# Optimization experiments

Hardware: AMD Instinct MI355X
Metric: run time of the kernel (lower is better)

## Reference

```python
import jax, jax.numpy as jnp
import numpy as np

N, K, F, NRBF = 10000, 32, 128, 300
GAMMA = 10.0


def ssp(x):
    # shifted softplus: softplus(x) - log(2)
    return jax.nn.softplus(x) - jnp.log(2.0).astype(x.dtype)


def setup_inputs() -> dict:
    key = jax.random.key(0)
    ks = jax.random.split(key, 12)
    s = lambda fan_in: 1.0 / np.sqrt(fan_in)
    inp = {
        "xyz": jax.random.normal(ks[0], (N, 3), jnp.float32) * 5.0,
        "atomic": jax.random.normal(ks[1], (N, F), jnp.float32),
        "edge_mask": (jax.random.uniform(ks[2], (N, K)) < 0.9).astype(jnp.float32),
        "src": jax.random.randint(ks[3], (N, K), 0, N),
        # pre_conv Linear(F, F) with bias
        "W_pre": jax.random.uniform(ks[4], (F, F), jnp.float32, -s(F), s(F)),
        "b_pre": jax.random.uniform(ks[5], (F,), jnp.float32, -s(F), s(F)),
        # cfconv: Linear(300, F, bias=False), SSP, Linear(F, F, bias=False), SSP
        "W_cf1": jax.random.uniform(ks[6], (NRBF, F), jnp.float32, -s(NRBF), s(NRBF)),
        "W_cf2": jax.random.uniform(ks[7], (F, F), jnp.float32, -s(F), s(F)),
        # post_conv: Linear(F,F), SSP, Linear(F,F)
        "W_post1": jax.random.uniform(ks[8], (F, F), jnp.float32, -s(F), s(F)),
        "b_post1": jax.random.uniform(ks[9], (F,), jnp.float32, -s(F), s(F)),
        "W_post2": jax.random.uniform(ks[10], (F, F), jnp.float32, -s(F), s(F)),
        "b_post2": jax.random.uniform(ks[11], (F,), jnp.float32, -s(F), s(F)),
        "rbf_centers": jnp.linspace(0.1, 30.1, NRBF, dtype=jnp.float32),
    }
    return inp


def reference(xyz, atomic, edge_mask, src, W_pre, b_pre, W_cf1, W_cf2,
              W_post1, b_post1, W_post2, b_post2, rbf_centers):
    pre = atomic @ W_pre + b_pre                       # [N, F]
    nbr_xyz = xyz[src]                                 # gather: [N, K, 3]
    d_ij = jnp.linalg.norm(nbr_xyz - xyz[:, None, :], axis=2, keepdims=True)  # [N, K, 1]
    rbf = jnp.exp(-GAMMA * (d_ij - rbf_centers[None, None, :]) ** 2)          # [N, K, 300]
    filters = ssp(ssp(rbf @ W_cf1) @ W_cf2)            # [N, K, F]
    conv_out = jnp.sum(filters * pre[src] * edge_mask[:, :, None], axis=1)    # [N, F]
    post = ssp(conv_out @ W_post1 + b_post1) @ W_post2 + b_post2
    return atomic + post
```

## Files before the change

### kernel.cpp

```cpp
#include <hip/hip_runtime.h>

#define NATOMS 10000
#define KNB 32
#define FD 128
#define NRBF 300
#define STEPC (30.0f / 299.0f)
#define INVSTEP (299.0f / 30.0f)
#define TROWS 256

typedef short short8 __attribute__((ext_vector_type(8)));
typedef float f32x4 __attribute__((ext_vector_type(4)));
typedef unsigned int u32x4 __attribute__((ext_vector_type(4)));

__device__ __forceinline__ unsigned short f2bf_rne(float f) {
    unsigned int u = __float_as_uint(f);
    u = (u + 0x7fffu + ((u >> 16) & 1u)) >> 16;
    return (unsigned short)u;
}

__device__ __forceinline__ unsigned int pack_bf2(float hi, float lo) {
    return __builtin_amdgcn_perm(__float_as_uint(hi) + 0x8000u,
                                 __float_as_uint(lo) + 0x8000u, 0x07060302u);
}

__device__ __forceinline__ unsigned short f2bf_rhu(float f) {
    return (unsigned short)((__float_as_uint(f) + 0x8000u) >> 16);
}

__device__ __forceinline__ float ssp_fast(float x) {
    float t = __builtin_amdgcn_exp2f(x * 1.44269504f);
    float l = __builtin_amdgcn_logf(1.0f + t);
    return 0.69314718056f * (l - 1.0f);
}

__device__ __forceinline__ float ssp_poly(float x) {
    float u = x * x;
    float p = fmaf(u, 2.1356923e-6f, -2.6351976e-5f);
    p = fmaf(u, p, 3.2552083e-4f);
    p = fmaf(u, p, -5.2083333e-3f);
    p = fmaf(u, p, 0.125f);
    return fmaf(0.5f, x, u * p);
}

__device__ __forceinline__ void gload_lds16(const void* g, void* l) {
    __builtin_amdgcn_global_load_lds(
        (const __attribute__((address_space(1))) unsigned int*)g,
        (__attribute__((address_space(3))) unsigned int*)l, 16, 0, 0);
}

__device__ __forceinline__ short8 rbf_row8(float d, float cg) {
    float t = d - cg;
    t = fminf(3.5f, fmaxf(-3.5f, t));
    float r = __builtin_amdgcn_exp2f(-14.4269504f * t * t);
    float q = __builtin_amdgcn_exp2f((28.8539008f * STEPC) * t
                                     - (14.4269504f * STEPC * STEPC));
    const float QRATIO = 0.81763172f;
    u32x4 p;
#pragma unroll
    for (int jj = 0; jj < 4; ++jj) {
        float v0 = r; r *= q; q *= QRATIO;
        float v1 = r; r *= q; q *= QRATIO;
        p[jj] = pack_bf2(v1, v0);
    }
    return __builtin_bit_cast(short8, p);
}

__global__ __launch_bounds__(256) void prep_pack(
    const float* __restrict__ Wcf1, const float* __restrict__ Wpre,
    const float* __restrict__ Wcf2, const float* __restrict__ Wpost1,
    const float* __restrict__ Wpost2, unsigned short* __restrict__ w1p,
    unsigned short* __restrict__ w4p) {
    int idx = blockIdx.x * 256 + threadIdx.x;
    if (idx < 40960) {
        int j = idx & 7, c = (idx >> 3) & 127, g = (idx >> 10) & 3, kc = idx >> 12;
        int k = kc * 32 + g * 8 + j;
        float v = (k < NRBF) ? Wcf1[k * FD + c] : 0.f;
        w1p[idx] = f2bf_rne(v);
    } else if (idx < 40960 + 65536) {
        int t = idx - 40960;
        int sel = t >> 14;
        int t2 = t & 16383;
        int j = t2 & 7, c = (t2 >> 3) & 127, g = (t2 >> 10) & 3, kc = t2 >> 12;
        int k = kc * 32 + g * 8 + j;
        const float* W = (sel == 0) ? Wpre : (sel == 1) ? Wcf2 : (sel == 2) ? Wpost1 : Wpost2;
        w4p[t] = f2bf_rne(W[k * FD + c]);
    }
}

__global__ __launch_bounds__(256) void pre_and_table(
    const float* __restrict__ X, const unsigned short* __restrict__ Wp,
    const float* __restrict__ bias, unsigned int* __restrict__ preP,
    const unsigned short* __restrict__ w1p, const unsigned short* __restrict__ w2p,
    unsigned int* __restrict__ T) {
    __shared__ unsigned short A2[128][132];
    const int tid = threadIdx.x;
    const int w = tid >> 6, lane = tid & 63, g = lane >> 4, c16 = lane & 15;

    if (blockIdx.x < 157) {
        const int r0 = blockIdx.x * 64 + w * 16;
        f32x4 acc[8];
#pragma unroll
        for (int b = 0; b < 8; ++b) acc[b] = (f32x4){0.f, 0.f, 0.f, 0.f};
        int row = r0 + c16;
        if (row >= NATOMS) row = 0;
#pragma unroll
        for (int kc = 0; kc < 4; ++kc) {
            const float* p0 = X + (size_t)row * FD + kc * 32 + g * 8;
            float4 xa = *(const float4*)p0, xb = *(const float4*)(p0 + 4);
            u32x4 pa;
            pa[0] = pack_bf2(xa.y, xa.x); pa[1] = pack_bf2(xa.w, xa.z);
            pa[2] = pack_bf2(xb.y, xb.x); pa[3] = pack_bf2(xb.w, xb.z);
            short8 a0 = __builtin_bit_cast(short8, pa);
            const unsigned short* wb = Wp + (kc * 4 + g) * 1024 + c16 * 8;
#pragma unroll
            for (int nb = 0; nb < 8; ++nb) {
                short8 b = *(const short8*)(wb + nb * 128);
                acc[nb] = __builtin_amdgcn_mfma_f32_16x16x32_bf16(a0, b, acc[nb], 0, 0, 0);
            }
        }
        float bv[8];
#pragma unroll
        for (int nb = 0; nb < 8; ++nb) bv[nb] = bias[nb * 16 + c16];
#pragma unroll
        for (int q = 0; q < 4; ++q) {
            int orow = r0 + 4 * g + q;
            if (orow < NATOMS) {
#pragma unroll
                for (int p2 = 0; p2 < 4; ++p2) {
                    float v0 = acc[2 * p2][q] + bv[2 * p2];
                    float v1 = acc[2 * p2 + 1][q] + bv[2 * p2 + 1];
                    preP[orow * 64 + c16 * 4 + p2] = pack_bf2(v1, v0);
                }
            }
        }
        return;
    }

    const int rbase = (int)(blockIdx.x - 157) * 128 + w * 32;
    const float hstep = 0.125f;
    const float d0 = (float)(rbase + c16) * hstep;
    const float d1 = (float)(rbase + 16 + c16) * hstep;

    const float BAND = 1.05f;
    float lo = (float)rbase * hstep, hi = (float)(rbase + 31) * hstep;
    int L = max(0, (int)floorf(((lo - BAND - 0.1f) * INVSTEP - 31.f) * 0.03125f));
    int H = min(9, (int)floorf(((hi + BAND - 0.1f) * INVSTEP) * 0.03125f));

    f32x4 acc[2][8];
#pragma unroll
    for (int a = 0; a < 2; ++a)
#pragma unroll
        for (int b = 0; b < 8; ++b) acc[a][b] = (f32x4){0.f, 0.f, 0.f, 0.f};

    for (int kc = L; kc <= H; ++kc) {
        const unsigned short* wb = w1p + kc * 4096 + g * 1024 + c16 * 8;
        short8 bfr[8];
#pragma unroll
        for (int nb = 0; nb < 8; ++nb) bfr[nb] = *(const short8*)(wb + nb * 128);
        const float cg = 0.1f + (float)(kc * 32 + g * 8) * STEPC;
        short8 a0 = rbf_row8(d0, cg);
        short8 a1 = rbf_row8(d1, cg);
#pragma unroll
        for (int nb = 0; nb < 8; ++nb) {
            acc[0][nb] = __builtin_amdgcn_mfma_f32_16x16x32_bf16(a0, bfr[nb], acc[0][nb], 0, 0, 0);
            acc[1][nb] = __builtin_amdgcn_mfma_f32_16x16x32_bf16(a1, bfr[nb], acc[1][nb], 0, 0, 0);
        }
    }

#pragma unroll
    for (int mr = 0; mr < 2; ++mr)
#pragma unroll
        for (int nb = 0; nb < 8; ++nb)
#pragma unroll
            for (int q = 0; q < 4; ++q) {
                int row = w * 32 + mr * 16 + 4 * g + q;
                A2[row][nb * 16 + c16] = f2bf_rhu(ssp_poly(acc[mr][nb][q]));
            }

    f32x4 acc2[2][8];
#pragma unroll
    for (int a = 0; a < 2; ++a)
#pragma unroll
        for (int b = 0; b < 8; ++b) acc2[a][b] = (f32x4){0.f, 0.f, 0.f, 0.f};

#pragma unroll
    for (int kc = 0; kc < 4; ++kc) {
        short8 a0 = *(const short8*)&A2[w * 32 + c16][kc * 32 + g * 8];
        short8 a1 = *(const short8*)&A2[w * 32 + 16 + c16][kc * 32 + g * 8];
        const unsigned short* wb = w2p + (kc * 4 + g) * 1024 + c16 * 8;
#pragma unroll
        for (int nb = 0; nb < 8; ++nb) {
            short8 b = *(const short8*)(wb + nb * 128);
            acc2[0][nb] = __builtin_amdgcn_mfma_f32_16x16x32_bf16(a0, b, acc2[0][nb], 0, 0, 0);
            acc2[1][nb] = __builtin_amdgcn_mfma_f32_16x16x32_bf16(a1, b, acc2[1][nb], 0, 0, 0);
        }
    }

#pragma unroll
    for (int mr = 0; mr < 2; ++mr)
#pragma unroll
        for (int q = 0; q < 4; ++q) {
            int r = rbase + mr * 16 + 4 * g + q;
#pragma unroll
            for (int p2 = 0; p2 < 4; ++p2) {
                float F0 = ssp_poly(acc2[mr][2 * p2][q]);
                float F1 = ssp_poly(acc2[mr][2 * p2 + 1][q]);
                T[r * 64 + c16 * 4 + p2] =
                    ((unsigned int)f2bf_rne(F1) << 16) | f2bf_rne(F0);
            }
        }
}

__global__ __launch_bounds__(512) void conv_kernel(
    const float* __restrict__ xyz, const int* __restrict__ src,
    const float* __restrict__ mask, const unsigned int* __restrict__ preP,
    const unsigned int* __restrict__ T, float* __restrict__ conv) {
    __shared__ unsigned int Tl[TROWS * 64];
    const int tid = threadIdx.x;
    const int w = tid >> 6;
    const int lane = tid & 63;
    const int l5 = lane & 31;

#pragma unroll
    for (int it = 0; it < 8; ++it) {
        const unsigned int* gp = T + w * 2048 + it * 256 + lane * 4;
        gload_lds16(gp, &Tl[w * 2048 + it * 256]);
    }
    __syncthreads();

#pragma unroll
    for (int rnd = 0; rnd < 2; ++rnd) {
        const int i = blockIdx.x * 16 + rnd * 8 + w;

        int sv = src[i * KNB + l5];
        float mv = mask[i * KNB + l5];
        float dx = xyz[3 * sv]     - xyz[3 * i];
        float dy = xyz[3 * sv + 1] - xyz[3 * i + 1];
        float dz = xyz[3 * sv + 2] - xyz[3 * i + 2];
        float dk = sqrtf(dx * dx + dy * dy + dz * dz);
        dk = (mv > 0.f) ? dk : 1e9f;
        float t = fminf(dk * 8.0f, (float)(TROWS - 2) + 0.999f);
        float fi = floorf(t);
        float fr = t - fi;
        int ii = (int)fi;

        float a0 = 0.f, a1 = 0.f;
#pragma unroll
        for (int e = 0; e < KNB; ++e) {
            int   ie = __builtin_amdgcn_readlane(ii, e);
            int   se = __builtin_amdgcn_readlane(sv, e);
            float fe = __uint_as_float((unsigned int)__builtin_amdgcn_readlane(
                           (int)__float_as_uint(fr), e));
            unsigned int tvA = Tl[ie * 64 + lane];
            unsigned int tvB = Tl[ie * 64 + 64 + lane];
            unsigned int pw = preP[se * 64 + lane];
            float A0 = __uint_as_float(tvA << 16);
            float A1 = __uint_as_float(tvA & 0xffff0000u);
            float B0 = __uint_as_float(tvB << 16);
            float B1 = __uint_as_float(tvB & 0xffff0000u);
            float f0 = fmaf(fe, B0 - A0, A0);
            float f1 = fmaf(fe, B1 - A1, A1);
            a0 = fmaf(f0, __uint_as_float(pw << 16), a0);
            a1 = fmaf(f1, __uint_as_float(pw & 0xffff0000u), a1);
        }
        int c0 = 32 * (lane & 3) + (lane >> 2);
        conv[i * FD + c0] = a0;
        conv[i * FD + c0 + 16] = a1;
    }
}

__global__ __launch_bounds__(256) void post_fused(
    const float* __restrict__ X, const unsigned short* __restrict__ w1,
    const float* __restrict__ b1, const unsigned short* __restrict__ w2,
    const float* __restrict__ b2, const float* __restrict__ resid,
    float* __restrict__ Y) {
    __shared__ unsigned short A2[32][132];
    const int tid = threadIdx.x;
    const int wv = tid >> 6, lane = tid & 63, g = lane >> 4, c16 = lane & 15;
    const int r = wv >> 1;
    const int c = wv & 1;
    const int r0 = blockIdx.x * 32 + r * 16;

    f32x4 acc[4];
#pragma unroll
    for (int b = 0; b < 4; ++b) acc[b] = (f32x4){0.f, 0.f, 0.f, 0.f};

    int row = r0 + c16;
    if (row >= NATOMS) row = 0;

#pragma unroll
    for (int kc = 0; kc < 4; ++kc) {
        const float* p0 = X + (size_t)row * FD + kc * 32 + g * 8;
        float4 xa = *(const float4*)p0, xb = *(const float4*)(p0 + 4);
        u32x4 pa;
        pa[0] = pack_bf2(xa.y, xa.x); pa[1] = pack_bf2(xa.w, xa.z);
        pa[2] = pack_bf2(xb.y, xb.x); pa[3] = pack_bf2(xb.w, xb.z);
        short8 a0 = __builtin_bit_cast(short8, pa);
        const unsigned short* wb = w1 + (kc * 4 + g) * 1024;
#pragma unroll
        for (int nb = 0; nb < 4; ++nb) {
            short8 b = *(const short8*)(wb + ((c * 4 + nb) * 16 + c16) * 8);
            acc[nb] = __builtin_amdgcn_mfma_f32_16x16x32_bf16(a0, b, acc[nb], 0, 0, 0);
        }
    }

#pragma unroll
    for (int nb = 0; nb < 4; ++nb) {
        float bv = b1[(c * 4 + nb) * 16 + c16];
#pragma unroll
        for (int q = 0; q < 4; ++q)
            A2[r * 16 + 4 * g + q][(c * 4 + nb) * 16 + c16] =
                f2bf_rhu(ssp_fast(acc[nb][q] + bv));
    }
    __syncthreads();

    f32x4 acc2[4];
#pragma unroll
    for (int b = 0; b < 4; ++b) acc2[b] = (f32x4){0.f, 0.f, 0.f, 0.f};

#pragma unroll
    for (int kc = 0; kc < 4; ++kc) {
        short8 a0 = *(const short8*)&A2[r * 16 + c16][kc * 32 + g * 8];
        const unsigned short* wb = w2 + (kc * 4 + g) * 1024;
#pragma unroll
        for (int nb = 0; nb < 4; ++nb) {
            short8 b = *(const short8*)(wb + ((c * 4 + nb) * 16 + c16) * 8);
            acc2[nb] = __builtin_amdgcn_mfma_f32_16x16x32_bf16(a0, b, acc2[nb], 0, 0, 0);
        }
    }

#pragma unroll
    for (int q = 0; q < 4; ++q) {
        int orow = r0 + 4 * g + q;
        if (orow < NATOMS) {
#pragma unroll
            for (int nb = 0; nb < 4; ++nb) {
                int o = orow * FD + (c * 4 + nb) * 16 + c16;
                Y[o] = acc2[nb][q] + b2[(c * 4 + nb) * 16 + c16] + resid[o];
            }
        }
    }
}

extern "C" void kernel_launch(void* const* d_in, const int* in_sizes, int n_in,
                              void* d_out, int out_size, void* d_ws, size_t ws_size,
                              hipStream_t stream) {
    const float* xyz     = (const float*)d_in[0];
    const float* atomic  = (const float*)d_in[1];
    const float* mask    = (const float*)d_in[2];
    const int*   src     = (const int*)d_in[3];
    const float* W_pre   = (const float*)d_in[4];
    const float* b_pre   = (const float*)d_in[5];
    const float* W_cf1   = (const float*)d_in[6];
    const float* W_cf2   = (const float*)d_in[7];
    const float* W_post1 = (const float*)d_in[8];
    const float* b_post1 = (const float*)d_in[9];
    const float* W_post2 = (const float*)d_in[10];
    const float* b_post2 = (const float*)d_in[11];
    float* out = (float*)d_out;

    unsigned int*   preP = (unsigned int*)d_ws;
    float*          conv = (float*)((char*)d_ws + 2560000);
    unsigned short* w1p  = (unsigned short*)((char*)d_ws + 7680000);
    unsigned short* w4p  = w1p + 40960;
    unsigned int*   T    = (unsigned int*)((char*)d_ws + 7892992);
    unsigned short* wpre   = w4p;
    unsigned short* wcf2   = w4p + 16384;
    unsigned short* wpost1 = w4p + 32768;
    unsigned short* wpost2 = w4p + 49152;

    prep_pack<<<416, 256, 0, stream>>>(W_cf1, W_pre, W_cf2, W_post1, W_post2, w1p, w4p);
    pre_and_table<<<159, 256, 0, stream>>>(atomic, wpre, b_pre, preP, w1p, wcf2, T);
    conv_kernel<<<625, 512, 0, stream>>>(xyz, src, mask, preP, T, conv);
    post_fused<<<313, 256, 0, stream>>>(conv, wpost1, b_post1, wpost2, b_post2, atomic, out);
}
```

Measured before the change: 44.87 us.

## Fuse conv aggregation with post MLP into one kernel via LDS

```diff
diff --git a/kernel.cpp b/kernel.cpp
--- a/kernel.cpp
+++ b/kernel.cpp
@@ -211,32 +211,39 @@
         }
 }
 
-__global__ __launch_bounds__(512) void conv_kernel(
+__global__ __launch_bounds__(256, 2) void conv_post(
     const float* __restrict__ xyz, const int* __restrict__ src,
     const float* __restrict__ mask, const unsigned int* __restrict__ preP,
-    const unsigned int* __restrict__ T, float* __restrict__ conv) {
+    const unsigned int* __restrict__ T, const unsigned short* __restrict__ w1,
+    const float* __restrict__ b1, const unsigned short* __restrict__ w2,
+    const float* __restrict__ b2, const float* __restrict__ resid,
+    float* __restrict__ Y) {
     __shared__ unsigned int Tl[TROWS * 64];
+    __shared__ unsigned short Aconv[32][132];
+
     const int tid = threadIdx.x;
     const int w = tid >> 6;
     const int lane = tid & 63;
     const int l5 = lane & 31;
-
-#pragma unroll
-    for (int it = 0; it < 8; ++it) {
-        const unsigned int* gp = T + w * 2048 + it * 256 + lane * 4;
-        gload_lds16(gp, &Tl[w * 2048 + it * 256]);
+    const int c16 = lane & 15;
+    const int g = lane >> 4;
+
+#pragma unroll
+    for (int it = 0; it < 16; ++it) {
+        const unsigned int* gp = T + w * 4096 + it * 256 + lane * 4;
+        gload_lds16(gp, &Tl[w * 4096 + it * 256]);
     }
     __syncthreads();
 
-#pragma unroll
-    for (int rnd = 0; rnd < 2; ++rnd) {
-        const int i = blockIdx.x * 16 + rnd * 8 + w;
-
-        int sv = src[i * KNB + l5];
-        float mv = mask[i * KNB + l5];
-        float dx = xyz[3 * sv]     - xyz[3 * i];
-        float dy = xyz[3 * sv + 1] - xyz[3 * i + 1];
-        float dz = xyz[3 * sv + 2] - xyz[3 * i + 2];
+    for (int a = 0; a < 8; ++a) {
+        int i = blockIdx.x * 32 + w * 8 + a;
+        int i2 = (i < NATOMS) ? i : 0;
+
+        int sv = src[i2 * KNB + l5];
+        float mv = mask[i2 * KNB + l5];
+        float dx = xyz[3 * sv]     - xyz[3 * i2];
+        float dy = xyz[3 * sv + 1] - xyz[3 * i2 + 1];
+        float dz = xyz[3 * sv + 2] - xyz[3 * i2 + 2];
         float dk = sqrtf(dx * dx + dy * dy + dz * dz);
         dk = (mv > 0.f) ? dk : 1e9f;
         float t = fminf(dk * 8.0f, (float)(TROWS - 2) + 0.999f);
@@ -264,38 +271,23 @@
             a1 = fmaf(f1, __uint_as_float(pw & 0xffff0000u), a1);
         }
         int c0 = 32 * (lane & 3) + (lane >> 2);
-        conv[i * FD + c0] = a0;
-        conv[i * FD + c0 + 16] = a1;
-    }
-}
-
-__global__ __launch_bounds__(256) void post_fused(
-    const float* __restrict__ X, const unsigned short* __restrict__ w1,
-    const float* __restrict__ b1, const unsigned short* __restrict__ w2,
-    const float* __restrict__ b2, const float* __restrict__ resid,
-    float* __restrict__ Y) {
-    __shared__ unsigned short A2[32][132];
-    const int tid = threadIdx.x;
-    const int wv = tid >> 6, lane = tid & 63, g = lane >> 4, c16 = lane & 15;
-    const int r = wv >> 1;
-    const int c = wv & 1;
+        Aconv[w * 8 + a][c0]      = f2bf_rhu(a0);
+        Aconv[w * 8 + a][c0 + 16] = f2bf_rhu(a1);
+    }
+    __syncthreads();
+
+    unsigned short* Amid = (unsigned short*)Tl;
+    const int r = w >> 1;
+    const int c = w & 1;
     const int r0 = blockIdx.x * 32 + r * 16;
 
     f32x4 acc[4];
 #pragma unroll
     for (int b = 0; b < 4; ++b) acc[b] = (f32x4){0.f, 0.f, 0.f, 0.f};
 
-    int row = r0 + c16;
-    if (row >= NATOMS) row = 0;
-
 #pragma unroll
     for (int kc = 0; kc < 4; ++kc) {
-        const float* p0 = X + (size_t)row * FD + kc * 32 + g * 8;
-        float4 xa = *(const float4*)p0, xb = *(const float4*)(p0 + 4);
-        u32x4 pa;
-        pa[0] = pack_bf2(xa.y, xa.x); pa[1] = pack_bf2(xa.w, xa.z);
-        pa[2] = pack_bf2(xb.y, xb.x); pa[3] = pack_bf2(xb.w, xb.z);
-        short8 a0 = __builtin_bit_cast(short8, pa);
+        short8 a0 = *(const short8*)&Aconv[r * 16 + c16][kc * 32 + g * 8];
         const unsigned short* wb = w1 + (kc * 4 + g) * 1024;
 #pragma unroll
         for (int nb = 0; nb < 4; ++nb) {
@@ -309,7 +301,7 @@
         float bv = b1[(c * 4 + nb) * 16 + c16];
 #pragma unroll
         for (int q = 0; q < 4; ++q)
-            A2[r * 16 + 4 * g + q][(c * 4 + nb) * 16 + c16] =
+            Amid[(r * 16 + 4 * g + q) * 132 + (c * 4 + nb) * 16 + c16] =
                 f2bf_rhu(ssp_fast(acc[nb][q] + bv));
     }
     __syncthreads();
@@ -320,7 +312,7 @@
 
 #pragma unroll
     for (int kc = 0; kc < 4; ++kc) {
-        short8 a0 = *(const short8*)&A2[r * 16 + c16][kc * 32 + g * 8];
+        short8 a0 = *(const short8*)&Amid[(r * 16 + c16) * 132 + kc * 32 + g * 8];
         const unsigned short* wb = w2 + (kc * 4 + g) * 1024;
 #pragma unroll
         for (int nb = 0; nb < 4; ++nb) {
@@ -360,7 +352,6 @@
     float* out = (float*)d_out;
 
     unsigned int*   preP = (unsigned int*)d_ws;
-    float*          conv = (float*)((char*)d_ws + 2560000);
     unsigned short* w1p  = (unsigned short*)((char*)d_ws + 7680000);
     unsigned short* w4p  = w1p + 40960;
     unsigned int*   T    = (unsigned int*)((char*)d_ws + 7892992);
@@ -371,6 +362,6 @@
 
     prep_pack<<<416, 256, 0, stream>>>(W_cf1, W_pre, W_cf2, W_post1, W_post2, w1p, w4p);
     pre_and_table<<<159, 256, 0, stream>>>(atomic, wpre, b_pre, preP, w1p, wcf2, T);
-    conv_kernel<<<625, 512, 0, stream>>>(xyz, src, mask, preP, T, conv);
-    post_fused<<<313, 256, 0, stream>>>(conv, wpost1, b_post1, wpost2, b_post2, atomic, out);
-}
+    conv_post<<<313, 256, 0, stream>>>(xyz, src, mask, preP, T,
+                                       wpost1, b_post1, wpost2, b_post2, atomic, out);
+}
```

After: 48.13 us. +7.3%, slower.
